# Performance work log

Hardware: AMD Instinct MI355X
Metric: run time of the kernel (lower is better)

## Reference

```python
import jax, jax.numpy as jnp
import numpy as np

N = 2048          # num agents / graph nodes
D = 128           # n_actor == n_map
ALPHA = 0.2       # GAT leakyrelu alpha
NEG = -1e9
X_IDX = [4, 9, 14, 19]   # actors_inter_cat time indices per LSTM step
E_IDX = [0, 4, 9, 14]    # graph_adjs time indices per LSTM step


def setup_inputs() -> dict:
    key = jax.random.key(0)
    ks = jax.random.split(key, 10)
    xavier = lambda k, shape: jax.random.uniform(
        k, shape, jnp.float32, -1.0, 1.0) * 1.414 * np.sqrt(6.0 / (shape[-2] + shape[-1]))
    actors_inter_cat = jax.random.normal(ks[0], (N, 20, D), jnp.float32)
    graph_adjs = jax.random.randint(ks[1], (N, 20, N), 0, 2, jnp.int32)
    # 4 GAT_SRF gates (forget, input, input_cell, output), stacked on leading axis
    Wg = xavier(ks[2], (4, 2 * D, D))          # gate projection W: in=2*D, out=D
    ag = xavier(ks[3], (4, 2 * D))             # attention vector a (2*out_features,)
    W = xavier(ks[4], (D, D))                  # GAT cell output projection
    b = xavier(ks[5], (1, D))
    h0 = xavier(ks[6], (1, D))
    conv_w = jax.random.normal(ks[7], (3, D, D, 2), jnp.float32) * (1.0 / np.sqrt(2 * D))
    conv_b = jax.random.normal(ks[8], (3, D), jnp.float32) * 0.01
    return {"actors_inter_cat": actors_inter_cat, "graph_adjs": graph_adjs,
            "Wg": Wg, "ag": ag, "W": W, "b": b, "h0": h0,
            "conv_w": conv_w, "conv_b": conv_b}


def _gat_gates(gin, mask, Wg, ag):
    # gin: (N, 2D); mask: (N, N) bool. Computes all 4 GAT_SRF gates at once.
    Wh = jnp.einsum('nf,gfo->gno', gin, Wg)                 # (4, N, D)
    s_src = jnp.einsum('gno,go->gn', Wh, ag[:, :D])         # a^T [Wh_i ..]
    s_dst = jnp.einsum('gno,go->gn', Wh, ag[:, D:])
    e = jax.nn.leaky_relu(s_src[:, :, None] + s_dst[:, None, :], ALPHA)  # (4,N,N)
    e = jnp.where(mask[None], e, NEG)
    attn = jax.nn.softmax(e, axis=-1)
    return jax.nn.elu(jnp.einsum('gnm,gmo->gno', attn, Wh))  # concat=True -> ELU


def reference(actors_inter_cat, graph_adjs, Wg, ag, W, b, h0, conv_w, conv_b):
    n = actors_inter_cat.shape[0]
    cell = actors_inter_cat[:, 0, :]
    hidden = jnp.broadcast_to(h0, (n, D))
    outs = []
    for t in range(4):  # fixed 4-step recurrence
        X = actors_inter_cat[:, X_IDX[t], :]
        mask = graph_adjs[:, E_IDX[t], :] > 0
        gin = jnp.concatenate([X, hidden], axis=1)          # (N, 2D)
        g = _gat_gates(gin, mask, Wg, ag)                   # (4, N, D)
        forget = jax.nn.sigmoid(g[0])
        inp_gate = jax.nn.sigmoid(g[1])
        inp_cell = jnp.tanh(g[2])
        out_gate = jax.nn.sigmoid(g[3])
        cell = cell * forget + inp_gate * inp_cell
        hidden = jnp.tanh(cell) * out_gate
        outs.append(jax.nn.sigmoid(hidden @ W + b))
    y = jnp.stack(outs, axis=2)                             # (N, D, 4)
    for l in range(3):  # kernel-2 Conv1d stack: length 4 -> 3 -> 2 -> 1
        y = (jnp.einsum('nct,oc->not', y[:, :, :-1], conv_w[l, :, :, 0])
             + jnp.einsum('nct,oc->not', y[:, :, 1:], conv_w[l, :, :, 1])
             + conv_b[l][None, :, None])
    return y[:, :, 0]                                       # squeeze -> (N, D)
```

## Files before the change

### kernel.cpp

```cpp
#include <hip/hip_runtime.h>

typedef __attribute__((ext_vector_type(8))) short short8;
typedef __attribute__((ext_vector_type(4))) float floatx4;

#define MFMA16(a,b,c) __builtin_amdgcn_mfma_f32_16x16x32_bf16(a,b,c,0,0,0)

__device__ __forceinline__ unsigned short f2bf(float f){
  unsigned u = __float_as_uint(f);
  u += 0x7fffu + ((u >> 16) & 1u);
  return (unsigned short)(u >> 16);
}
__device__ __forceinline__ float sigm(float x){ return 1.f/(1.f+__expf(-x)); }

__global__ __launch_bounds__(256) void init_kernel(const float* __restrict__ actors,
    const float* __restrict__ h0, unsigned short* __restrict__ hbf, float* __restrict__ cell){
  int idx = blockIdx.x*256 + threadIdx.x;
  int n = idx >> 7, c = idx & 127;
  hbf[idx]  = f2bf(h0[c]);
  cell[idx] = actors[(size_t)n*2560 + c];
}

__global__ __launch_bounds__(256) void wgt_kernel(const float* __restrict__ Wg,
    unsigned short* __restrict__ WgT){
  int e = blockIdx.x*256 + threadIdx.x;
  int g = e >> 15, o = (e >> 8) & 127, f = e & 255;
  WgT[(size_t)g*32768 + o*256 + f] = f2bf(Wg[(size_t)g*32768 + f*128 + o]);
}

__global__ __launch_bounds__(256) void cwt_kernel(const float* __restrict__ cw,
    float* __restrict__ cwT){
  int e = blockIdx.x*256 + threadIdx.x;
  int l = e >> 14, r = e & 16383, k = r >> 7, o = r & 127;
  cwT[(size_t)l*32768 + k*256 + o]       = cw[(size_t)l*32768 + o*256 + k*2];
  cwT[(size_t)l*32768 + k*256 + 128 + o] = cw[(size_t)l*32768 + o*256 + k*2 + 1];
}

__global__ __launch_bounds__(256) void mask_kernel(const int* __restrict__ adj,
    unsigned long long* __restrict__ bm){
  const int E[4] = {0,4,9,14};
  int t = blockIdx.y;
  int wv = threadIdx.x >> 6, lane = threadIdx.x & 63;
  int n = blockIdx.x*4 + wv;
  const int* row = adj + (size_t)n*40960 + (size_t)E[t]*2048;
  unsigned long long* outp = bm + ((size_t)t*2048 + n)*32;
  for (int it=0; it<32; ++it){
    unsigned long long bal = __ballot(row[it*64 + lane] > 0);
    if (lane == 0) outp[it] = bal;
  }
}

__global__ __launch_bounds__(256) void whgemm_kernel(const float* __restrict__ actors,
    const unsigned short* __restrict__ hbf, const unsigned short* __restrict__ WgT,
    const float* __restrict__ ag, unsigned short* __restrict__ WhT,
    float* __restrict__ s_src, float* __restrict__ s_dst, int xoff){
  __shared__ __align__(16) unsigned short ginb[32*264];
  __shared__ float sred[4][2][32];
  int g = blockIdx.y, n0 = blockIdx.x*32, tid = threadIdx.x;
  {
    int row = tid >> 3, q = tid & 7;
    if (q < 4){
      const float4* src = (const float4*)(actors + (size_t)(n0+row)*2560 + xoff + q*32);
      unsigned short* dst = &ginb[row*264 + q*32];
      #pragma unroll
      for (int j=0;j<4;++j){
        float4 a = src[2*j], b = src[2*j+1];
        unsigned short tmp[8] = {f2bf(a.x),f2bf(a.y),f2bf(a.z),f2bf(a.w),
                                 f2bf(b.x),f2bf(b.y),f2bf(b.z),f2bf(b.w)};
        *(uint4*)(dst + j*8) = *(const uint4*)tmp;
      }
    } else {
      const uint4* src = (const uint4*)(hbf + (size_t)(n0+row)*128 + (q-4)*32);
      uint4* dst = (uint4*)&ginb[row*264 + 128 + (q-4)*32];
      #pragma unroll
      for (int j=0;j<4;++j) dst[j] = src[j];
    }
  }
  __syncthreads();
  int wv = tid>>6, lane = tid&63, quad = lane>>4, l16 = lane&15;
  int ob = wv*32;
  floatx4 acc[2][2];
  #pragma unroll
  for (int i=0;i<2;++i) for (int j=0;j<2;++j) acc[i][j] = (floatx4){0.f,0.f,0.f,0.f};
  const unsigned short* wga = WgT + (size_t)g*32768;
  #pragma unroll
  for (int kh=0; kh<8; ++kh){
    int k = kh*32 + quad*8;
    short8 a0 = *(const short8*)(wga + (size_t)(ob + l16)*256 + k);
    short8 a1 = *(const short8*)(wga + (size_t)(ob + 16 + l16)*256 + k);
    #pragma unroll
    for (int j=0;j<2;++j){
      short8 b = *(const short8*)&ginb[(j*16 + l16)*264 + k];
      acc[0][j] = MFMA16(a0, b, acc[0][j]);
      acc[1][j] = MFMA16(a1, b, acc[1][j]);
    }
  }
  float agS[2][4], agD[2][4];
  #pragma unroll
  for (int i=0;i<2;++i)
    #pragma unroll
    for (int r=0;r<4;++r){
      int o = ob + i*16 + quad*4 + r;
      agS[i][r] = ag[g*256 + o];
      agD[i][r] = ag[g*256 + 128 + o];
    }
  unsigned short* wht = WhT + (size_t)g*262144;
  float psrc[2], pdst[2];
  #pragma unroll
  for (int j=0;j<2;++j){
    float ps = 0.f, pd = 0.f;
    #pragma unroll
    for (int i=0;i<2;++i)
      #pragma unroll
      for (int r=0;r<4;++r){
        float v = acc[i][j][r];
        ps += v*agS[i][r]; pd += v*agD[i][r];
        wht[(size_t)(ob + i*16 + quad*4 + r)*2048 + n0 + j*16 + l16] = f2bf(v);
      }
    psrc[j] = ps; pdst[j] = pd;
  }
  #pragma unroll
  for (int j=0;j<2;++j){
    psrc[j] += __shfl_down(psrc[j], 16); psrc[j] += __shfl_down(psrc[j], 32);
    pdst[j] += __shfl_down(pdst[j], 16); pdst[j] += __shfl_down(pdst[j], 32);
  }
  if (quad == 0){
    #pragma unroll
    for (int j=0;j<2;++j){
      sred[wv][0][j*16+l16] = psrc[j];
      sred[wv][1][j*16+l16] = pdst[j];
    }
  }
  __syncthreads();
  if (tid < 64){
    int which = tid>>5, n = tid&31;
    float s = sred[0][which][n]+sred[1][which][n]+sred[2][which][n]+sred[3][which][n];
    (which ? s_dst : s_src)[g*2048 + n0 + n] = s;
  }
}

__global__ __launch_bounds__(512) void attn_kernel(const unsigned long long* __restrict__ bm,
    const unsigned short* __restrict__ WhT, const float* __restrict__ s_src,
    const float* __restrict__ s_dst, float* __restrict__ gout, int t){
  __shared__ __align__(16) char lds_raw[94336];
  int g = blockIdx.y, n0 = blockIdx.x*32, tid = threadIdx.x;
  int wv = tid>>6, lane = tid&63, quad = lane>>4, l16 = lane&15;
  int grp = tid>>7, gtid = tid&127, ow = wv&1;
  unsigned short* whs = (unsigned short*)(lds_raw + grp*18432);
  unsigned short* Ps  = (unsigned short*)(lds_raw + 73728 + grp*4608);
  float* zpart = (float*)(lds_raw + 92160);
  float* zrow  = (float*)(lds_raw + 94208);
  float* obufA = (float*)(lds_raw);
  float* obufB = (float*)(lds_raw + 16896);

  const unsigned short* whg = WhT + (size_t)g*262144 + (size_t)gtid*2048;
  int prow = gtid>>2, pseg = gtid&3;
  float srcv = s_src[g*2048 + n0 + prow];
  const unsigned long long* mrow = bm + ((size_t)t*2048 + n0 + prow)*32;
  const float* sd = s_dst + g*2048;
  float z_acc = 0.f;
  floatx4 acc[2][4];
  #pragma unroll
  for (int i=0;i<2;++i) for (int j=0;j<4;++j) acc[i][j] = (floatx4){0.f,0.f,0.f,0.f};

  for (int c=0; c<8; ++c){
    int m0 = grp*512 + c*64;
    __syncthreads();
    {
      const uint4* src = (const uint4*)(whg + m0);
      uint4 v[8];
      #pragma unroll
      for (int j=0;j<8;++j) v[j] = src[j];
      uint4* dst = (uint4*)(whs + gtid*72);
      #pragma unroll
      for (int j=0;j<8;++j) dst[j] = v[j];
    }
    {
      unsigned long long mw = mrow[grp*8 + c];
      unsigned short mb = (unsigned short)(mw >> (pseg*16));
      const float4* sd4 = (const float4*)(sd + m0 + pseg*16);
      float4 s0 = sd4[0], s1 = sd4[1], s2 = sd4[2], s3 = sd4[3];
      float sv[16] = {s0.x,s0.y,s0.z,s0.w, s1.x,s1.y,s1.z,s1.w,
                      s2.x,s2.y,s2.z,s2.w, s3.x,s3.y,s3.z,s3.w};
      unsigned short us[16];
      #pragma unroll
      for (int j=0;j<16;++j){
        float s = srcv + sv[j];
        s = s > 0.f ? s : 0.2f*s;
        float p = ((mb >> j) & 1) ? __expf(s) : 0.f;
        z_acc += p;
        us[j] = f2bf(p);
      }
      uint4* pd = (uint4*)(Ps + prow*72 + pseg*16);
      pd[0] = *(const uint4*)us;
      pd[1] = *(const uint4*)(us+8);
    }
    __syncthreads();
    #pragma unroll
    for (int kh=0; kh<2; ++kh){
      int kc = kh*32 + quad*8;
      short8 a0 = *(const short8*)(Ps + l16*72 + kc);
      short8 a1 = *(const short8*)(Ps + (16+l16)*72 + kc);
      #pragma unroll
      for (int j=0;j<4;++j){
        short8 b = *(const short8*)(whs + (size_t)(ow*64 + j*16 + l16)*72 + kc);
        acc[0][j] = MFMA16(a0, b, acc[0][j]);
        acc[1][j] = MFMA16(a1, b, acc[1][j]);
      }
    }
  }
  zpart[tid] = z_acc;
  __syncthreads();
  if (grp < 2){
    float* obx = (grp & 1) ? obufB : obufA;
    #pragma unroll
    for (int i=0;i<2;++i)
      #pragma unroll
      for (int j=0;j<4;++j)
        #pragma unroll
        for (int r=0;r<4;++r)
          obx[(i*16 + quad*4 + r)*132 + ow*64 + j*16 + l16] = acc[i][j][r];
  }
  __syncthreads();
  if (tid < 32){
    float s = 0.f;
    #pragma unroll
    for (int k=0;k<16;++k) s += zpart[(k>>2)*128 + tid*4 + (k&3)];
    zrow[tid] = s;
  }
  if (grp >= 2){
    float* obx = (grp & 1) ? obufB : obufA;
    #pragma unroll
    for (int i=0;i<2;++i)
      #pragma unroll
      for (int j=0;j<4;++j)
        #pragma unroll
        for (int r=0;r<4;++r)
          obx[(i*16 + quad*4 + r)*132 + ow*64 + j*16 + l16] += acc[i][j][r];
  }
  __syncthreads();
  {
    int row = tid>>4, c0 = (tid&15)*8;
    float inv = 1.f / zrow[row];
    float* go = gout + (size_t)g*262144 + (size_t)(n0+row)*128 + c0;
    #pragma unroll
    for (int j=0;j<8;++j){
      float v = (obufA[row*132 + c0 + j] + obufB[row*132 + c0 + j]) * inv;
      go[j] = v > 0.f ? v : __expf(v) - 1.f;
    }
  }
}

__global__ __launch_bounds__(256) void gate_kernel(const float* __restrict__ gbuf,
    float* __restrict__ cell, unsigned short* __restrict__ hbf, const float* __restrict__ W,
    const float* __restrict__ b, float* __restrict__ y, int t){
  __shared__ float h[256];
  int tid = threadIdx.x;
  int r = tid >> 7, o = tid & 127;
  int n = blockIdx.x*2 + r;
  size_t idx = (size_t)n*128 + o;
  float g0 = gbuf[idx], g1 = gbuf[262144+idx], g2 = gbuf[524288+idx], g3 = gbuf[786432+idx];
  float fg = sigm(g0), ig = sigm(g1), ic = tanhf(g2), og = sigm(g3);
  float cl = cell[idx]*fg + ig*ic;
  float hd = tanhf(cl)*og;
  cell[idx] = cl; hbf[idx] = f2bf(hd);
  h[tid] = hd;
  __syncthreads();
  float acc = b[o];
  const float* hr = h + r*128;
  for (int k=0;k<128;++k) acc += hr[k]*W[k*128+o];
  y[(size_t)n*512 + o*4 + t] = sigm(acc);
}

template<int TIN, bool LAST>
__global__ __launch_bounds__(256) void conv_kernel(const float* __restrict__ yin,
    const float* __restrict__ cwT, const float* __restrict__ cb, float* __restrict__ yout, int l){
  __shared__ float ylds[2][128][4];
  int tid = threadIdx.x;
  int r = tid >> 7, o = tid & 127;
  int n = blockIdx.x*2 + r;
  float4 yv = *(const float4*)&yin[(size_t)n*512 + o*4];
  *(float4*)&ylds[r][o][0] = yv;
  __syncthreads();
  const float* w = cwT + (size_t)l*32768;
  float acc[TIN-1];
  #pragma unroll
  for (int j=0;j<TIN-1;++j) acc[j] = 0.f;
  for (int k=0;k<128;++k){
    float w0 = w[k*256 + o], w1 = w[k*256 + 128 + o];
    float y0 = ylds[r][k][0], y1 = ylds[r][k][1];
    acc[0] += y0*w0 + y1*w1;
    if (TIN > 2){
      float y2 = ylds[r][k][2];
      acc[1] += y1*w0 + y2*w1;
      if (TIN > 3){
        float y3 = ylds[r][k][3];
        acc[2] += y2*w0 + y3*w1;
      }
    }
  }
  float bb = cb[l*128 + o];
  if (LAST){
    yout[(size_t)n*128 + o] = acc[0] + bb;
  } else {
    #pragma unroll
    for (int tt=0; tt<TIN-1; ++tt) yout[(size_t)n*512 + o*4 + tt] = acc[tt] + bb;
  }
}

extern "C" void kernel_launch(void* const* d_in, const int* in_sizes, int n_in,
                              void* d_out, int out_size, void* d_ws, size_t ws_size,
                              hipStream_t stream) {
  const float* actors = (const float*)d_in[0];
  const int*   adj    = (const int*)d_in[1];
  const float* Wg     = (const float*)d_in[2];
  const float* ag     = (const float*)d_in[3];
  const float* W      = (const float*)d_in[4];
  const float* b      = (const float*)d_in[5];
  const float* h0     = (const float*)d_in[6];
  const float* cw     = (const float*)d_in[7];
  const float* cb     = (const float*)d_in[8];
  float* out = (float*)d_out;

  char* ws = (char*)d_ws;
  unsigned long long* bm = (unsigned long long*)ws;
  float* cell          = (float*)(ws + (size_t)(2u<<20));
  unsigned short* hbf  = (unsigned short*)(ws + (size_t)(3u<<20));
  unsigned short* WgT  = (unsigned short*)(ws + (size_t)3670016);
  float* s_src         = (float*)(ws + (size_t)3932160);
  float* s_dst         = (float*)(ws + (size_t)3932160 + 32768);
  unsigned short* WhT  = (unsigned short*)(ws + (size_t)(4u<<20));
  float* cwT           = (float*)(ws + (size_t)(6u<<20));
  float* gbuf          = (float*)(ws + (size_t)(7u<<20));
  float* yA            = (float*)(ws + (size_t)(11u<<20));
  float* yB            = (float*)(ws + (size_t)(15u<<20));

  const int XI[4] = {4, 9, 14, 19};

  init_kernel<<<1024, 256, 0, stream>>>(actors, h0, hbf, cell);
  wgt_kernel<<<512, 256, 0, stream>>>(Wg, WgT);
  cwt_kernel<<<192, 256, 0, stream>>>(cw, cwT);
  mask_kernel<<<dim3(512,4), 256, 0, stream>>>(adj, bm);
  for (int t=0; t<4; ++t){
    whgemm_kernel<<<dim3(64,4), 256, 0, stream>>>(actors, hbf, WgT, ag, WhT, s_src, s_dst, XI[t]*128);
    attn_kernel  <<<dim3(64,4), 512, 0, stream>>>(bm, WhT, s_src, s_dst, gbuf, t);
    gate_kernel  <<<1024, 256, 0, stream>>>(gbuf, cell, hbf, W, b, yA, t);
  }
  conv_kernel<4,false><<<1024, 256, 0, stream>>>(yA, cwT, cb, yB, 0);
  conv_kernel<3,false><<<1024, 256, 0, stream>>>(yB, cwT, cb, yA, 1);
  conv_kernel<2,true> <<<1024, 256, 0, stream>>>(yA, cwT, cb, out, 2);
}
```

Measured before the change: 654.7 us.

## Fuse prep and conv kernels; restructure attention to read Wh directly from global

Merges the four setup kernels into one prep kernel with block-range dispatch, and fuses the three Conv1d layers into one kernel that keeps intermediates in LDS. The attention kernel now uses 16-row tiles (twice the blocks) and builds MFMA operands straight from registers, loading Wh B-fragments from global/L2 instead of staging them through LDS with barriers. This cuts launch overhead, LDS traffic and syncs, but the attention B loads are strided global reads that may have poorer locality.

```diff
diff --git a/kernel.cpp b/kernel.cpp
--- a/kernel.cpp
+++ b/kernel.cpp
@@ -12,40 +12,37 @@
 }
 __device__ __forceinline__ float sigm(float x){ return 1.f/(1.f+__expf(-x)); }
 
-__global__ __launch_bounds__(256) void init_kernel(const float* __restrict__ actors,
-    const float* __restrict__ h0, unsigned short* __restrict__ hbf, float* __restrict__ cell){
-  int idx = blockIdx.x*256 + threadIdx.x;
-  int n = idx >> 7, c = idx & 127;
-  hbf[idx]  = f2bf(h0[c]);
-  cell[idx] = actors[(size_t)n*2560 + c];
-}
-
-__global__ __launch_bounds__(256) void wgt_kernel(const float* __restrict__ Wg,
-    unsigned short* __restrict__ WgT){
-  int e = blockIdx.x*256 + threadIdx.x;
-  int g = e >> 15, o = (e >> 8) & 127, f = e & 255;
-  WgT[(size_t)g*32768 + o*256 + f] = f2bf(Wg[(size_t)g*32768 + f*128 + o]);
-}
-
-__global__ __launch_bounds__(256) void cwt_kernel(const float* __restrict__ cw,
-    float* __restrict__ cwT){
-  int e = blockIdx.x*256 + threadIdx.x;
-  int l = e >> 14, r = e & 16383, k = r >> 7, o = r & 127;
-  cwT[(size_t)l*32768 + k*256 + o]       = cw[(size_t)l*32768 + o*256 + k*2];
-  cwT[(size_t)l*32768 + k*256 + 128 + o] = cw[(size_t)l*32768 + o*256 + k*2 + 1];
-}
-
-__global__ __launch_bounds__(256) void mask_kernel(const int* __restrict__ adj,
-    unsigned long long* __restrict__ bm){
-  const int E[4] = {0,4,9,14};
-  int t = blockIdx.y;
-  int wv = threadIdx.x >> 6, lane = threadIdx.x & 63;
-  int n = blockIdx.x*4 + wv;
-  const int* row = adj + (size_t)n*40960 + (size_t)E[t]*2048;
-  unsigned long long* outp = bm + ((size_t)t*2048 + n)*32;
-  for (int it=0; it<32; ++it){
-    unsigned long long bal = __ballot(row[it*64 + lane] > 0);
-    if (lane == 0) outp[it] = bal;
+__global__ __launch_bounds__(256) void prep_kernel(const float* __restrict__ actors,
+    const float* __restrict__ h0, const float* __restrict__ Wg, const float* __restrict__ cw,
+    const int* __restrict__ adj, unsigned short* __restrict__ hbf, float* __restrict__ cell,
+    unsigned short* __restrict__ WgT, float* __restrict__ cwT, unsigned long long* __restrict__ bm){
+  int bid = blockIdx.x;
+  if (bid < 1024){
+    int idx = bid*256 + threadIdx.x;
+    int n = idx >> 7, c = idx & 127;
+    hbf[idx]  = f2bf(h0[c]);
+    cell[idx] = actors[(size_t)n*2560 + c];
+  } else if (bid < 1536){
+    int e = (bid-1024)*256 + threadIdx.x;
+    int g = e >> 15, o = (e >> 8) & 127, f = e & 255;
+    WgT[(size_t)g*32768 + o*256 + f] = f2bf(Wg[(size_t)g*32768 + f*128 + o]);
+  } else if (bid < 1728){
+    int e = (bid-1536)*256 + threadIdx.x;
+    int l = e >> 14, rr = e & 16383, k = rr >> 7, o = rr & 127;
+    cwT[(size_t)l*32768 + k*256 + o]       = cw[(size_t)l*32768 + o*256 + k*2];
+    cwT[(size_t)l*32768 + k*256 + 128 + o] = cw[(size_t)l*32768 + o*256 + k*2 + 1];
+  } else {
+    const int E[4] = {0,4,9,14};
+    int mb = bid - 1728;
+    int t = mb & 3, nblk = mb >> 2;
+    int wv = threadIdx.x >> 6, lane = threadIdx.x & 63;
+    int n = nblk*4 + wv;
+    const int* row = adj + (size_t)n*40960 + (size_t)E[t]*2048;
+    unsigned long long* outp = bm + ((size_t)t*2048 + n)*32;
+    for (int it=0; it<32; ++it){
+      unsigned long long bal = __ballot(row[it*64 + lane] > 0);
+      if (lane == 0) outp[it] = bal;
+    }
   }
 }
 
@@ -138,113 +135,77 @@
   }
 }
 
-__global__ __launch_bounds__(512) void attn_kernel(const unsigned long long* __restrict__ bm,
+__global__ __launch_bounds__(512) void attn_kernel(const unsigned char* __restrict__ bmb,
     const unsigned short* __restrict__ WhT, const float* __restrict__ s_src,
     const float* __restrict__ s_dst, float* __restrict__ gout, int t){
-  __shared__ __align__(16) char lds_raw[94336];
-  int g = blockIdx.y, n0 = blockIdx.x*32, tid = threadIdx.x;
-  int wv = tid>>6, lane = tid&63, quad = lane>>4, l16 = lane&15;
-  int grp = tid>>7, gtid = tid&127, ow = wv&1;
-  unsigned short* whs = (unsigned short*)(lds_raw + grp*18432);
-  unsigned short* Ps  = (unsigned short*)(lds_raw + 73728 + grp*4608);
-  float* zpart = (float*)(lds_raw + 92160);
-  float* zrow  = (float*)(lds_raw + 94208);
-  float* obufA = (float*)(lds_raw);
-  float* obufB = (float*)(lds_raw + 16896);
-
-  const unsigned short* whg = WhT + (size_t)g*262144 + (size_t)gtid*2048;
-  int prow = gtid>>2, pseg = gtid&3;
-  float srcv = s_src[g*2048 + n0 + prow];
-  const unsigned long long* mrow = bm + ((size_t)t*2048 + n0 + prow)*32;
+  __shared__ float obuf[2][2][16][72];
+  __shared__ float zpart[4][16];
+  __shared__ float zrow[16];
+  int g = blockIdx.y, n0 = blockIdx.x*16, tid = threadIdx.x;
+  int w = tid>>6, lane = tid&63, quad = lane>>4, l16 = lane&15;
+  int ohalf = w & 1, mg = w >> 1;
+  const unsigned short* whg = WhT + (size_t)g*262144 + (size_t)(ohalf*64)*2048;
   const float* sd = s_dst + g*2048;
-  float z_acc = 0.f;
-  floatx4 acc[2][4];
-  #pragma unroll
-  for (int i=0;i<2;++i) for (int j=0;j<4;++j) acc[i][j] = (floatx4){0.f,0.f,0.f,0.f};
-
-  for (int c=0; c<8; ++c){
-    int m0 = grp*512 + c*64;
-    __syncthreads();
-    {
-      const uint4* src = (const uint4*)(whg + m0);
-      uint4 v[8];
-      #pragma unroll
-      for (int j=0;j<8;++j) v[j] = src[j];
-      uint4* dst = (uint4*)(whs + gtid*72);
-      #pragma unroll
-      for (int j=0;j<8;++j) dst[j] = v[j];
-    }
-    {
-      unsigned long long mw = mrow[grp*8 + c];
-      unsigned short mb = (unsigned short)(mw >> (pseg*16));
-      const float4* sd4 = (const float4*)(sd + m0 + pseg*16);
-      float4 s0 = sd4[0], s1 = sd4[1], s2 = sd4[2], s3 = sd4[3];
-      float sv[16] = {s0.x,s0.y,s0.z,s0.w, s1.x,s1.y,s1.z,s1.w,
-                      s2.x,s2.y,s2.z,s2.w, s3.x,s3.y,s3.z,s3.w};
-      unsigned short us[16];
-      #pragma unroll
-      for (int j=0;j<16;++j){
+  float srcv = s_src[g*2048 + n0 + l16];
+  const unsigned char* mr = bmb + ((size_t)t*2048 + n0 + l16)*256;
+  float z0 = 0.f;
+  floatx4 acc[4];
+  #pragma unroll
+  for (int j=0;j<4;++j) acc[j] = (floatx4){0.f,0.f,0.f,0.f};
+  for (int c=0;c<8;++c){
+    int mbase = mg*512 + c*64;
+    #pragma unroll
+    for (int kh=0; kh<2; ++kh){
+      int mk = mbase + kh*32 + quad*8;
+      float4 sda = *(const float4*)(sd + mk);
+      float4 sdb = *(const float4*)(sd + mk + 4);
+      unsigned mb = mr[mk>>3];
+      float sv[8] = {sda.x,sda.y,sda.z,sda.w,sdb.x,sdb.y,sdb.z,sdb.w};
+      short8 a0;
+      #pragma unroll
+      for (int j=0;j<8;++j){
         float s = srcv + sv[j];
         s = s > 0.f ? s : 0.2f*s;
-        float p = ((mb >> j) & 1) ? __expf(s) : 0.f;
-        z_acc += p;
-        us[j] = f2bf(p);
+        float p = ((mb >> j) & 1u) ? __expf(s) : 0.f;
+        z0 += p;
+        a0[j] = (short)f2bf(p);
       }
-      uint4* pd = (uint4*)(Ps + prow*72 + pseg*16);
-      pd[0] = *(const uint4*)us;
-      pd[1] = *(const uint4*)(us+8);
-    }
-    __syncthreads();
-    #pragma unroll
-    for (int kh=0; kh<2; ++kh){
-      int kc = kh*32 + quad*8;
-      short8 a0 = *(const short8*)(Ps + l16*72 + kc);
-      short8 a1 = *(const short8*)(Ps + (16+l16)*72 + kc);
+      const unsigned short* bp = whg + mk;
       #pragma unroll
       for (int j=0;j<4;++j){
-        short8 b = *(const short8*)(whs + (size_t)(ow*64 + j*16 + l16)*72 + kc);
-        acc[0][j] = MFMA16(a0, b, acc[0][j]);
-        acc[1][j] = MFMA16(a1, b, acc[1][j]);
+        short8 b = *(const short8*)(bp + (size_t)(j*16 + l16)*2048);
+        acc[j] = MFMA16(a0, b, acc[j]);
       }
     }
   }
-  zpart[tid] = z_acc;
-  __syncthreads();
-  if (grp < 2){
-    float* obx = (grp & 1) ? obufB : obufA;
-    #pragma unroll
-    for (int i=0;i<2;++i)
-      #pragma unroll
-      for (int j=0;j<4;++j)
-        #pragma unroll
-        for (int r=0;r<4;++r)
-          obx[(i*16 + quad*4 + r)*132 + ow*64 + j*16 + l16] = acc[i][j][r];
-  }
-  __syncthreads();
-  if (tid < 32){
-    float s = 0.f;
-    #pragma unroll
-    for (int k=0;k<16;++k) s += zpart[(k>>2)*128 + tid*4 + (k&3)];
-    zrow[tid] = s;
-  }
-  if (grp >= 2){
-    float* obx = (grp & 1) ? obufB : obufA;
-    #pragma unroll
-    for (int i=0;i<2;++i)
-      #pragma unroll
-      for (int j=0;j<4;++j)
-        #pragma unroll
-        for (int r=0;r<4;++r)
-          obx[(i*16 + quad*4 + r)*132 + ow*64 + j*16 + l16] += acc[i][j][r];
-  }
-  __syncthreads();
-  {
-    int row = tid>>4, c0 = (tid&15)*8;
+  z0 += __shfl_down(z0, 32);
+  z0 += __shfl_down(z0, 16);
+  if (ohalf == 0 && lane < 16) zpart[mg][l16] = z0;
+  if (mg < 2){
+    #pragma unroll
+    for (int j=0;j<4;++j)
+      #pragma unroll
+      for (int r=0;r<4;++r)
+        obuf[ohalf][mg][quad*4+r][j*16+l16] = acc[j][r];
+  }
+  __syncthreads();
+  if (mg >= 2){
+    #pragma unroll
+    for (int j=0;j<4;++j)
+      #pragma unroll
+      for (int r=0;r<4;++r)
+        obuf[ohalf][mg-2][quad*4+r][j*16+l16] += acc[j][r];
+  }
+  if (tid < 16) zrow[tid] = zpart[0][tid]+zpart[1][tid]+zpart[2][tid]+zpart[3][tid];
+  __syncthreads();
+  {
+    int row = tid>>5, c0 = (tid&31)*4;
+    int half = c0>>6, oc = c0&63;
     float inv = 1.f / zrow[row];
     float* go = gout + (size_t)g*262144 + (size_t)(n0+row)*128 + c0;
     #pragma unroll
-    for (int j=0;j<8;++j){
-      float v = (obufA[row*132 + c0 + j] + obufB[row*132 + c0 + j]) * inv;
+    for (int j=0;j<4;++j){
+      float v = (obuf[half][0][row][oc+j] + obuf[half][1][row][oc+j]) * inv;
       go[j] = v > 0.f ? v : __expf(v) - 1.f;
     }
   }
@@ -271,39 +232,48 @@
   y[(size_t)n*512 + o*4 + t] = sigm(acc);
 }
 
-template<int TIN, bool LAST>
-__global__ __launch_bounds__(256) void conv_kernel(const float* __restrict__ yin,
-    const float* __restrict__ cwT, const float* __restrict__ cb, float* __restrict__ yout, int l){
+__global__ __launch_bounds__(256) void convfused_kernel(const float* __restrict__ yin,
+    const float* __restrict__ cwT, const float* __restrict__ cb, float* __restrict__ out){
   __shared__ float ylds[2][128][4];
   int tid = threadIdx.x;
   int r = tid >> 7, o = tid & 127;
   int n = blockIdx.x*2 + r;
-  float4 yv = *(const float4*)&yin[(size_t)n*512 + o*4];
-  *(float4*)&ylds[r][o][0] = yv;
-  __syncthreads();
-  const float* w = cwT + (size_t)l*32768;
-  float acc[TIN-1];
-  #pragma unroll
-  for (int j=0;j<TIN-1;++j) acc[j] = 0.f;
-  for (int k=0;k<128;++k){
-    float w0 = w[k*256 + o], w1 = w[k*256 + 128 + o];
-    float y0 = ylds[r][k][0], y1 = ylds[r][k][1];
-    acc[0] += y0*w0 + y1*w1;
-    if (TIN > 2){
-      float y2 = ylds[r][k][2];
-      acc[1] += y1*w0 + y2*w1;
-      if (TIN > 3){
-        float y3 = ylds[r][k][3];
-        acc[2] += y2*w0 + y3*w1;
-      }
-    }
-  }
-  float bb = cb[l*128 + o];
-  if (LAST){
-    yout[(size_t)n*128 + o] = acc[0] + bb;
-  } else {
-    #pragma unroll
-    for (int tt=0; tt<TIN-1; ++tt) yout[(size_t)n*512 + o*4 + tt] = acc[tt] + bb;
+  *(float4*)&ylds[r][o][0] = *(const float4*)&yin[(size_t)n*512 + o*4];
+  __syncthreads();
+  {
+    const float* w = cwT;
+    float a0=0.f, a1=0.f, a2=0.f;
+    for (int k=0;k<128;++k){
+      float w0 = w[k*256 + o], w1 = w[k*256 + 128 + o];
+      float y0 = ylds[r][k][0], y1 = ylds[r][k][1], y2 = ylds[r][k][2], y3 = ylds[r][k][3];
+      a0 += y0*w0 + y1*w1; a1 += y1*w0 + y2*w1; a2 += y2*w0 + y3*w1;
+    }
+    float bb = cb[o];
+    __syncthreads();
+    ylds[r][o][0] = a0+bb; ylds[r][o][1] = a1+bb; ylds[r][o][2] = a2+bb;
+    __syncthreads();
+  }
+  {
+    const float* w = cwT + 32768;
+    float a0=0.f, a1=0.f;
+    for (int k=0;k<128;++k){
+      float w0 = w[k*256 + o], w1 = w[k*256 + 128 + o];
+      float y0 = ylds[r][k][0], y1 = ylds[r][k][1], y2 = ylds[r][k][2];
+      a0 += y0*w0 + y1*w1; a1 += y1*w0 + y2*w1;
+    }
+    float bb = cb[128 + o];
+    __syncthreads();
+    ylds[r][o][0] = a0+bb; ylds[r][o][1] = a1+bb;
+    __syncthreads();
+  }
+  {
+    const float* w = cwT + 65536;
+    float a0=0.f;
+    for (int k=0;k<128;++k){
+      float w0 = w[k*256 + o], w1 = w[k*256 + 128 + o];
+      a0 += ylds[r][k][0]*w0 + ylds[r][k][1]*w1;
+    }
+    out[(size_t)n*128 + o] = a0 + cb[256 + o];
   }
 }
 
@@ -332,20 +302,14 @@
   float* cwT           = (float*)(ws + (size_t)(6u<<20));
   float* gbuf          = (float*)(ws + (size_t)(7u<<20));
   float* yA            = (float*)(ws + (size_t)(11u<<20));
-  float* yB            = (float*)(ws + (size_t)(15u<<20));
 
   const int XI[4] = {4, 9, 14, 19};
 
-  init_kernel<<<1024, 256, 0, stream>>>(actors, h0, hbf, cell);
-  wgt_kernel<<<512, 256, 0, stream>>>(Wg, WgT);
-  cwt_kernel<<<192, 256, 0, stream>>>(cw, cwT);
-  mask_kernel<<<dim3(512,4), 256, 0, stream>>>(adj, bm);
+  prep_kernel<<<3776, 256, 0, stream>>>(actors, h0, Wg, cw, adj, hbf, cell, WgT, cwT, bm);
   for (int t=0; t<4; ++t){
     whgemm_kernel<<<dim3(64,4), 256, 0, stream>>>(actors, hbf, WgT, ag, WhT, s_src, s_dst, XI[t]*128);
-    attn_kernel  <<<dim3(64,4), 512, 0, stream>>>(bm, WhT, s_src, s_dst, gbuf, t);
+    attn_kernel  <<<dim3(128,4), 512, 0, stream>>>((const unsigned char*)bm, WhT, s_src, s_dst, gbuf, t);
     gate_kernel  <<<1024, 256, 0, stream>>>(gbuf, cell, hbf, W, b, yA, t);
   }
-  conv_kernel<4,false><<<1024, 256, 0, stream>>>(yA, cwT, cb, yB, 0);
-  conv_kernel<3,false><<<1024, 256, 0, stream>>>(yB, cwT, cb, yA, 1);
-  conv_kernel<2,true> <<<1024, 256, 0, stream>>>(yA, cwT, cb, out, 2);
-}
+  convfused_kernel<<<1024, 256, 0, stream>>>(yA, cwT, cb, out);
+}
```

New measurement: 674.5 us. +3.0%, slower.
